# Kernel tuning notes

Hardware: AMD Instinct MI355X
Metric: run time of the kernel (lower is better)

The kernel has to match this reference:

```python
import jax, jax.numpy as jnp
import numpy as np

B, T, D = 4, 4096, 384
H = W = 64
K = 8            # num_clusters
CH = MH = 64     # conv_hidden, mlp_hidden
NL = 4           # num_layers
IN_DIM = D + 2   # use_spatial_pos
RADIUS_FRACTION = 30.0
GRAPH_EPS = 1e-6
SM_LAMBDA = 0.01
FS_LAMBDA = 0.09


def conv2d(x, w, b, groups=1):
    out = jax.lax.conv_general_dilated(x, w, (1, 1), 'SAME',
        dimension_numbers=('NCHW', 'OIHW', 'NCHW'), feature_group_count=groups)
    return out + b[None, :, None, None]


def group_norm(x, g, b, groups, eps=1e-5):
    n, c, h, w = x.shape
    xg = x.reshape(n, groups, c // groups, h, w)
    m = xg.mean(axis=(2, 3, 4), keepdims=True)
    v = xg.var(axis=(2, 3, 4), keepdims=True)
    xn = ((xg - m) * jax.lax.rsqrt(v + eps)).reshape(n, c, h, w)
    return xn * g[None, :, None, None] + b[None, :, None, None]


def layer_norm(x, g, b, eps=1e-5):
    m = x.mean(-1, keepdims=True)
    v = x.var(-1, keepdims=True)
    return (x - m) * jax.lax.rsqrt(v + eps) * g + b


def build_graph():
    # unit-square grid positions; radius graph with self loops; sym normalization
    lin = jnp.linspace(0.0, 1.0, H)
    gy, gx = jnp.meshgrid(lin, lin, indexing='ij')
    pos = jnp.stack([gx.reshape(-1), gy.reshape(-1)], axis=1)  # (T,2)
    r2 = 2.0 / (RADIUS_FRACTION * RADIUS_FRACTION)             # (sqrt(2)/rf)^2
    dx = pos[:, 0][:, None] - pos[:, 0][None, :]
    dy = pos[:, 1][:, None] - pos[:, 1][None, :]
    adj = ((dx * dx + dy * dy) <= r2).astype(jnp.float32)      # includes loop
    deg = adj.sum(1)
    dis = jnp.where(deg > 0, deg ** -0.5, 0.0)
    a_tilde = dis[:, None] * adj * dis[None, :]                # D^-1/2 A D^-1/2
    return pos, a_tilde


def setup_inputs():
    key = jax.random.key(0)
    ks = jax.random.split(key, 16)
    rn = lambda i, s, sc=0.05: jax.random.normal(ks[i], s, dtype=jnp.float32) * sc
    z = lambda s: jnp.zeros(s, jnp.float32)
    o = lambda s: jnp.ones(s, jnp.float32)
    return {
        'token_features': jax.random.normal(ks[0], (B, T, D), dtype=jnp.float32),
        'gcn_w0': rn(1, (IN_DIM, CH)), 'gcn_b0': z((CH,)),
        'gcn_w': rn(2, (NL - 1, CH, CH)), 'gcn_b': z((NL - 1, CH)),
        'ln_g': o((NL, CH)), 'ln_b': z((NL, CH)),
        'res_w': rn(3, (IN_DIM, CH)), 'res_b': z((CH,)),
        'res_ln_g': o((CH,)), 'res_ln_b': z((CH,)),
        'mlp_w1': rn(4, (CH, MH)), 'mlp_b1': z((MH,)),
        'mlp_ln_g': o((MH,)), 'mlp_ln_b': z((MH,)),
        'mlp_w2': rn(5, (MH, K)), 'mlp_b2': z((K,)),
        'sm_w1': rn(6, (K, 1, 3, 3)), 'sm_b1': z((K,)),
        'sm_gn1_g': o((K,)), 'sm_gn1_b': z((K,)),
        'sm_w2': rn(7, (K, 1, 3, 3)), 'sm_b2': z((K,)),
        'sm_gn2_g': o((K,)), 'sm_gn2_b': z((K,)),
        'ec_w1': rn(8, (32, D, 3, 3), 0.02), 'ec_b1': z((32,)),
        'ec_gn_g': o((32,)), 'ec_gn_b': z((32,)),
        'ec_w2': rn(9, (1, 32, 1, 1)), 'ec_b2': z((1,)),
        'k': 8,
    }


def reference(token_features, gcn_w0, gcn_b0, gcn_w, gcn_b, ln_g, ln_b,
              res_w, res_b, res_ln_g, res_ln_b, mlp_w1, mlp_b1, mlp_ln_g,
              mlp_ln_b, mlp_w2, mlp_b2, sm_w1, sm_b1, sm_gn1_g, sm_gn1_b,
              sm_w2, sm_b2, sm_gn2_g, sm_gn2_b, ec_w1, ec_b1, ec_gn_g,
              ec_gn_b, ec_w2, ec_b2, k):
    pos, A = build_graph()

    # ---- feature smoothness loss (edge-aware) ----
    fs = token_features.reshape(B, H, W, D).transpose(0, 3, 1, 2)  # (B,D,H,W)
    e = jax.nn.relu(group_norm(conv2d(fs, ec_w1, ec_b1), ec_gn_g, ec_gn_b, 8))
    ew = jax.nn.sigmoid(conv2d(e, ec_w2, ec_b2))                   # (B,1,H,W)
    gy = fs[:, :, 1:, :] - fs[:, :, :-1, :]
    gx = fs[:, :, :, 1:] - fs[:, :, :, :-1]
    loss_y = (gy * gy * ew[:, :, 1:, :]).mean() / D
    loss_x = (gx * gx * ew[:, :, :, 1:]).mean() / D
    feat_sm = (loss_y + loss_x) / 2

    # ---- GNN pool (batched; adjacency shared across batch) ----
    x = jnp.concatenate(
        [token_features, jnp.broadcast_to(pos[None], (B, T, 2))], axis=-1)
    Ws = [gcn_w0] + [gcn_w[i] for i in range(NL - 1)]
    bs = [gcn_b0] + [gcn_b[i] for i in range(NL - 1)]
    for i in range(NL):
        x_prev = x
        h = jnp.einsum('ts,bsc->btc', A, x @ Ws[i]) + bs[i]  # GCNConv
        h = jax.nn.elu(layer_norm(h, ln_g[i], ln_b[i]))
        if i == 0:
            x_prev = layer_norm(x_prev @ res_w + res_b, res_ln_g, res_ln_b)
        x = h + x_prev
    h1 = jax.nn.elu(layer_norm(x @ mlp_w1 + mlp_b1, mlp_ln_g, mlp_ln_b))
    S = jax.nn.softmax(h1 @ mlp_w2 + mlp_b2, axis=-1)        # (B,T,K)

    # ---- spatial smoothness loss (depthwise convs) ----
    S_sp = S.transpose(0, 2, 1).reshape(B, K, H, W)
    t = jax.nn.relu(group_norm(conv2d(S_sp, sm_w1, sm_b1, groups=K),
                               sm_gn1_g, sm_gn1_b, K))
    S_sm = group_norm(conv2d(t, sm_w2, sm_b2, groups=K), sm_gn2_g, sm_gn2_b, K)
    sm_loss = ((S_sm - S_sp) ** 2).mean(axis=(1, 2, 3))      # (B,)

    # ---- normalized-cut + orthogonality losses ----
    AS = jnp.einsum('ts,bsk->btk', A, S)
    num = jnp.einsum('btk,btk->b', S, AS)
    degA = A.sum(1)
    den = jnp.einsum('btk,t,btk->b', S, degA, S) + GRAPH_EPS
    loss_c = -num / den
    SS = jnp.einsum('btk,btl->bkl', S, S)
    ssn = jnp.sqrt((SS * SS).sum(axis=(1, 2)))
    eyeK = jnp.eye(K, dtype=jnp.float32)
    target = eyeK / (jnp.sqrt(jnp.float32(K)) + GRAPH_EPS)
    diff = SS / (ssn[:, None, None] + GRAPH_EPS) - target[None]
    loss_o = jnp.sqrt((diff * diff).sum(axis=(1, 2)))

    loss = (loss_c + loss_o + SM_LAMBDA * sm_loss).mean() + FS_LAMBDA * feat_sm
    return S, loss
```

## Files before the change

kernel.cpp:

```cpp
#include <hip/hip_runtime.h>
#include <hip/hip_bf16.h>


#define B_ 4
#define T_ 4096
#define D_ 384

typedef __attribute__((ext_vector_type(8))) short short8b;
typedef __attribute__((ext_vector_type(4))) float f32x4;

__device__ __forceinline__ float wred(float v) {
#pragma unroll
  for (int off = 32; off > 0; off >>= 1) v += __shfl_xor(v, off);
  return v;
}

__device__ __forceinline__ void wred2(float& a, float& b) {
#pragma unroll
  for (int off = 32; off > 0; off >>= 1) {
    a += __shfl_xor(a, off);
    b += __shfl_xor(b, off);
  }
}

__device__ __forceinline__ short bf16rne(float f) {
  unsigned u = __float_as_uint(f);
  unsigned r = (u + 0x7FFFu + ((u >> 16) & 1u)) >> 16;
  return (short)r;
}

__device__ __forceinline__ float uval(int i) {
  int c = (i < 2 ? i : 2) + ((63 - i) < 2 ? (63 - i) : 2) + 1;
  return rsqrtf((float)c);
}

__device__ __forceinline__ short8b cvt8(const float* src) {
  float4 f0 = *(const float4*)src;
  float4 f1 = *(const float4*)(src + 4);
  short8b v;
  v[0] = bf16rne(f0.x); v[1] = bf16rne(f0.y);
  v[2] = bf16rne(f0.z); v[3] = bf16rne(f0.w);
  v[4] = bf16rne(f1.x); v[5] = bf16rne(f1.y);
  v[6] = bf16rne(f1.z); v[7] = bf16rne(f1.w);
  return v;
}

struct PGcn {
  const float *feat, *ecw1, *w0, *resw, *resb, *resg, *reslb;
  const float *gw, *gb0, *gb, *lng, *lnb;
  const float *w1, *b1, *mlng, *mlnb, *w2, *b2;
  short *wq, *wb;
  float *accg, *xwA, *xwB, *xbuf, *resbuf, *S, *Sp;
};

struct PLoss {
  const float *S, *Sp;
  const float *smw1, *smb1, *smg1, *smbb1, *smw2, *smb2, *smg2, *smbb2;
  const float *feat;
  const short *wq;
  const float *ecb1;
  float *eraw, *accg;
  const float *gng, *gnb, *ecw2, *ecb2;
  float *ew, *outp;
};


__device__ __forceinline__ void prep_stage(int blk, int tid,
    const float* ecw1, const float* w0, const float* resw,
    short* wq, short* wb, float* accg) {
  if (blk == 0) {
    accg[tid] = 0.f;
    accg[tid + 256] = 0.f;
  }
  if (blk < 432) {
    int idx = blk * 256 + tid;
    int q = idx % 9;
    int rest = idx / 9;
    int d = rest % 384;
    int o = rest / 384;
    wq[((size_t)(q * 32 + o)) * 384 + d] = bf16rne(ecw1[idx]);
  } else {
    int u = (blk - 432) * 256 + tid;
    int l = u & 63, f = (u >> 6) & 7, s = u >> 9;
    int c = f * 16 + (l & 15);
    int k0 = s * 32 + ((l >> 4) << 3);
    const float* src = (c < 64) ? (w0 + c) : (resw + (c - 64));
    short8b v;
#pragma unroll
    for (int j = 0; j < 8; ++j) v[j] = bf16rne(src[(size_t)(k0 + j) * 64]);
    *(short8b*)(wb + (size_t)u * 8) = v;
  }
}

__device__ __forceinline__ void gemm0_stage(char* smem, int blk, int tid,
    const float* feat, const short* wb, const float* w0, const float* resw,
    const float* resb, const float* resg, const float* reslb,
    float* xw, float* res) {
  short8b* Ab8 = (short8b*)smem;
  short8b* Bb8 = (short8b*)(smem + 24576);
  int row0 = blk * 32;
#pragma unroll
  for (int it = 0; it < 6; ++it) {
    int u = it * 256 + tid;
    int l = u & 63, s = (u >> 6) % 12, set = u / 768;
    int row = row0 + set * 16 + (l & 15);
    int k = s * 32 + ((l >> 4) << 3);
    Ab8[(set * 12 + s) * 64 + l] = cvt8(feat + (size_t)row * 384 + k);
  }
  int wid = tid >> 6, lane = tid & 63;
  int rowset = wid & 1, colhalf = wid >> 1;
  const short8b* wb8 = (const short8b*)wb;
  f32x4 acc[4];
#pragma unroll
  for (int f = 0; f < 4; ++f) acc[f] = (f32x4){0.f, 0.f, 0.f, 0.f};
  for (int c = 0; c < 3; ++c) {
    __syncthreads();
#pragma unroll
    for (int it = 0; it < 8; ++it) {
      int u = it * 256 + tid;
      Bb8[u] = wb8[c * 2048 + u];
    }
    __syncthreads();
#pragma unroll
    for (int s = 0; s < 4; ++s) {
      short8b av = Ab8[(rowset * 12 + c * 4 + s) * 64 + lane];
#pragma unroll
      for (int f = 0; f < 4; ++f) {
        short8b bv = Bb8[(s * 8 + colhalf * 4 + f) * 64 + lane];
        acc[f] = __builtin_amdgcn_mfma_f32_16x16x32_bf16(av, bv, acc[f], 0, 0, 0);
      }
    }
  }
  int g = lane >> 4, ln = lane & 15;
  if (colhalf == 0) {
    float pw1[4], pw2[4];
#pragma unroll
    for (int f = 0; f < 4; ++f) {
      int c = f * 16 + ln;
      pw1[f] = w0[384 * 64 + c];
      pw2[f] = w0[385 * 64 + c];
    }
#pragma unroll
    for (int r = 0; r < 4; ++r) {
      int grow = row0 + rowset * 16 + g * 4 + r;
      int t = grow & (T_ - 1);
      float px = (float)(t & 63) * (1.f / 63.f);
      float py = (float)(t >> 6) * (1.f / 63.f);
#pragma unroll
      for (int f = 0; f < 4; ++f)
        xw[(size_t)grow * 64 + f * 16 + ln] = acc[f][r] + px * pw1[f] + py * pw2[f];
    }
  } else {
    float rw1[4], rw2[4], rb[4], rgam[4], rbet[4];
#pragma unroll
    for (int f = 0; f < 4; ++f) {
      int c = f * 16 + ln;
      rw1[f] = resw[384 * 64 + c];
      rw2[f] = resw[385 * 64 + c];
      rb[f] = resb[c]; rgam[f] = resg[c]; rbet[f] = reslb[c];
    }
#pragma unroll
    for (int r = 0; r < 4; ++r) {
      int grow = row0 + rowset * 16 + g * 4 + r;
      int t = grow & (T_ - 1);
      float px = (float)(t & 63) * (1.f / 63.f);
      float py = (float)(t >> 6) * (1.f / 63.f);
      float rv[4];
      float s1 = 0.f, s2 = 0.f;
#pragma unroll
      for (int f = 0; f < 4; ++f) {
        float v = acc[f][r] + px * rw1[f] + py * rw2[f] + rb[f];
        rv[f] = v;
        s1 += v;
        s2 = fmaf(v, v, s2);
      }
#pragma unroll
      for (int off = 1; off < 16; off <<= 1) {
        s1 += __shfl_xor(s1, off);
        s2 += __shfl_xor(s2, off);
      }
      float mean = s1 * (1.f / 64.f);
      float var = s2 * (1.f / 64.f) - mean * mean;
      float inv = rsqrtf(var + 1e-5f);
#pragma unroll
      for (int f = 0; f < 4; ++f)
        res[(size_t)grow * 64 + f * 16 + ln] =
            (rv[f] - mean) * inv * rgam[f] + rbet[f];
    }
  }
}

__device__ __forceinline__ void layer_stage(char* smem, int blk, int tid,
    const float* xw_in, const float* W, const float* bias, const float* lng,
    const float* lnb, const float* resid, float* xout, float* xw_out) {
  float* sx = (float*)smem;
  float* sW = (float*)(smem + 4096);
  int t0 = blk * 16;
  int b = t0 >> 12, i = (t0 >> 6) & 63;
  const float4* w4 = (const float4*)W;
  float4* sW4 = (float4*)sW;
#pragma unroll
  for (int l = 0; l < 4; ++l) sW4[tid + l * 256] = w4[tid + l * 256];
  int c = tid & 63, jg = tid >> 6;
  int jb = (t0 & 63) + jg * 4;
  float ui = uval(i);
  float acc[4];
#pragma unroll
  for (int m = 0; m < 4; ++m) acc[m] = 0.f;
  float uw[8];
#pragma unroll
  for (int d = 0; d < 8; ++d) {
    int jj = jb - 2 + d;
    uw[d] = (jj >= 0 && jj < 64) ? uval(jj) : 0.f;
  }
#pragma unroll
  for (int di = -2; di <= 2; ++di) {
    int ii = i + di;
    if (ii < 0 || ii > 63) continue;
    float wi = uval(ii);
    const float* src = xw_in + ((size_t)((b << 12) + (ii << 6))) * 64 + c;
    float v[8];
#pragma unroll
    for (int d = 0; d < 8; ++d) {
      int jj = jb - 2 + d;
      v[d] = (jj >= 0 && jj < 64) ? src[jj * 64] : 0.f;
    }
#pragma unroll
    for (int m = 0; m < 4; ++m) {
      float t = v[m] * uw[m] + v[m + 1] * uw[m + 1] + v[m + 2] * uw[m + 2] +
                v[m + 3] * uw[m + 3] + v[m + 4] * uw[m + 4];
      acc[m] = fmaf(wi, t, acc[m]);
    }
  }
  float bc = bias[c], gam = lng[c], bet = lnb[c];
#pragma unroll
  for (int m = 0; m < 4; ++m) {
    int lrow = jg * 4 + m;
    float h = ui * uval(jb + m) * acc[m] + bc;
    float s1 = h, s2 = h * h;
    wred2(s1, s2);
    float mean = s1 * (1.f / 64.f);
    float var = s2 * (1.f / 64.f) - mean * mean;
    float n = (h - mean) * rsqrtf(var + 1e-5f) * gam + bet;
    float e = n > 0.f ? n : (expf(n) - 1.f);
    float xv = e + resid[(size_t)(t0 + lrow) * 64 + c];
    xout[(size_t)(t0 + lrow) * 64 + c] = xv;
    sx[lrow * 64 + c] = xv;
  }
  __syncthreads();
  float a[4];
#pragma unroll
  for (int m = 0; m < 4; ++m) a[m] = 0.f;
#pragma unroll
  for (int kq = 0; kq < 16; ++kq) {
    float4 fv[4];
#pragma unroll
    for (int m = 0; m < 4; ++m)
      fv[m] = *(const float4*)&sx[(jg * 4 + m) * 64 + kq * 4];
#pragma unroll
    for (int dk = 0; dk < 4; ++dk) {
      float wv = sW[(kq * 4 + dk) * 64 + c];
#pragma unroll
      for (int m = 0; m < 4; ++m)
        a[m] = fmaf(((const float*)&fv[m])[dk], wv, a[m]);
    }
  }
#pragma unroll
  for (int m = 0; m < 4; ++m)
    xw_out[(size_t)(t0 + jg * 4 + m) * 64 + c] = a[m];
}

__device__ __forceinline__ void st4mlp_stage(char* smem, int blk, int tid,
    const float* xw_in, const float* bias, const float* lng, const float* lnb,
    const float* resid, const float* w1, const float* b1, const float* mlng,
    const float* mlnb, const float* w2, const float* b2, float* S, float* Sp) {
  float* sx = (float*)smem;
  float* sW = (float*)(smem + 8192);
  float* sh = (float*)(smem + 24576);
  int t0 = blk * 32;
  int b = t0 >> 12, i = (t0 >> 6) & 63;
  const float4* w4 = (const float4*)w1;
  float4* sW4 = (float4*)sW;
#pragma unroll
  for (int l = 0; l < 4; ++l) sW4[tid + l * 256] = w4[tid + l * 256];
  int c = tid & 63, jg = tid >> 6;
  int jb = (t0 & 63) + jg * 8;
  float ui = uval(i);
  float acc[8];
#pragma unroll
  for (int m = 0; m < 8; ++m) acc[m] = 0.f;
  float uw[12];
#pragma unroll
  for (int d = 0; d < 12; ++d) {
    int jj = jb - 2 + d;
    uw[d] = (jj >= 0 && jj < 64) ? uval(jj) : 0.f;
  }
#pragma unroll
  for (int di = -2; di <= 2; ++di) {
    int ii = i + di;
    if (ii < 0 || ii > 63) continue;
    float wi = uval(ii);
    const float* src = xw_in + ((size_t)((b << 12) + (ii << 6))) * 64 + c;
    float v[12];
#pragma unroll
    for (int d = 0; d < 12; ++d) {
      int jj = jb - 2 + d;
      v[d] = (jj >= 0 && jj < 64) ? src[jj * 64] : 0.f;
    }
#pragma unroll
    for (int m = 0; m < 8; ++m) {
      float t = v[m] * uw[m] + v[m + 1] * uw[m + 1] + v[m + 2] * uw[m + 2] +
                v[m + 3] * uw[m + 3] + v[m + 4] * uw[m + 4];
      acc[m] = fmaf(wi, t, acc[m]);
    }
  }
  float bc = bias[c], gam = lng[c], bet = lnb[c];
#pragma unroll
  for (int m = 0; m < 8; ++m) {
    int lrow = jg * 8 + m;
    float h = ui * uval(jb + m) * acc[m] + bc;
    float s1 = h, s2 = h * h;
    wred2(s1, s2);
    float mean = s1 * (1.f / 64.f);
    float var = s2 * (1.f / 64.f) - mean * mean;
    float n = (h - mean) * rsqrtf(var + 1e-5f) * gam + bet;
    float e = n > 0.f ? n : (expf(n) - 1.f);
    sx[lrow * 64 + c] = e + resid[(size_t)(t0 + lrow) * 64 + c];
  }
  __syncthreads();
  float a[8];
#pragma unroll
  for (int m = 0; m < 8; ++m) a[m] = 0.f;
#pragma unroll
  for (int kq = 0; kq < 16; ++kq) {
    float4 fv[8];
#pragma unroll
    for (int m = 0; m < 8; ++m)
      fv[m] = *(const float4*)&sx[(jg * 8 + m) * 64 + kq * 4];
#pragma unroll
    for (int dk = 0; dk < 4; ++dk) {
      float wv = sW[(kq * 4 + dk) * 64 + c];
#pragma unroll
      for (int m = 0; m < 8; ++m)
        a[m] = fmaf(((const float*)&fv[m])[dk], wv, a[m]);
    }
  }
  float mb = b1[c], mgam = mlng[c], mbet = mlnb[c];
#pragma unroll
  for (int m = 0; m < 8; ++m) {
    float h = a[m] + mb;
    float s1 = h, s2 = h * h;
    wred2(s1, s2);
    float mean = s1 * (1.f / 64.f);
    float var = s2 * (1.f / 64.f) - mean * mean;
    float n = (h - mean) * rsqrtf(var + 1e-5f) * mgam + mbet;
    sh[(jg * 8 + m) * 64 + c] = n > 0.f ? n : (expf(n) - 1.f);
  }
  __syncthreads();
  int k = tid & 7, j = tid >> 3;
  float lg = b2[k];
#pragma unroll 8
  for (int u = 0; u < 64; ++u) {
    int cc = (u + j * 8) & 63;
    lg = fmaf(sh[j * 64 + cc], w2[cc * 8 + k], lg);
  }
  float mx = lg;
  mx = fmaxf(mx, __shfl_xor(mx, 1));
  mx = fmaxf(mx, __shfl_xor(mx, 2));
  mx = fmaxf(mx, __shfl_xor(mx, 4));
  float ex = expf(lg - mx);
  float sum = ex;
  sum += __shfl_xor(sum, 1);
  sum += __shfl_xor(sum, 2);
  sum += __shfl_xor(sum, 4);
  float val = ex / sum;
  int grow = t0 + j;
  int t = grow & (T_ - 1);
  S[(size_t)grow * 8 + k] = val;
  Sp[((size_t)((b << 3) + k) << 12) + t] = val;
}

__device__ __forceinline__ void cut_stage(char* smem, int blk, int tid,
    const float* S, float* accg) {
  {
    int k = tid & 7;
    int tl = tid >> 3;
    int gid = blk * 32 + tl;
    int b = gid >> 12, t = gid & (T_ - 1);
    int i = t >> 6, j = t & 63;
    float ui = uval(i), uj = uval(j);
    float as = 0.f, sui = 0.f, suj = 0.f;
#pragma unroll
    for (int di = -2; di <= 2; ++di) {
      int ii = i + di;
      if (ii < 0 || ii > 63) continue;
      float wi = uval(ii);
      sui += wi;
#pragma unroll
      for (int dj = -2; dj <= 2; ++dj) {
        int jj = j + dj;
        if (jj < 0 || jj > 63) continue;
        as = fmaf(wi * uval(jj),
                  S[((size_t)((b << 12) + (ii << 6) + jj)) * 8 + k], as);
      }
    }
#pragma unroll
    for (int dj = -2; dj <= 2; ++dj) {
      int jj = j + dj;
      if (jj >= 0 && jj <= 63) suj += uval(jj);
    }
    as *= ui * uj;
    float sv = S[(size_t)gid * 8 + k];
    float degA = ui * uj * sui * suj;
    float numv = sv * as, denv = sv * sv * degA;
    wred2(numv, denv);
    float* lds = (float*)smem;
    int wid = tid >> 6, lane = tid & 63;
    if (lane == 0) { lds[wid * 2] = numv; lds[wid * 2 + 1] = denv; }
    __syncthreads();
    if (tid == 0) {
      int slot = b * 4 + (blk & 3);
      atomicAdd(&accg[slot], lds[0] + lds[2] + lds[4] + lds[6]);
      atomicAdd(&accg[16 + slot], lds[1] + lds[3] + lds[5] + lds[7]);
    }
  }
  if (blk < 32) {
    __syncthreads();
    int b = blk >> 3, chunk = blk & 7;
    int wid = tid >> 6, lane = tid & 63;
    int kk = lane >> 3, ll = lane & 7;
    int t0 = chunk * 512 + wid * 128;
    float a = 0.f;
    const float* Sb = S + ((size_t)b << 12) * 8;
    for (int it = 0; it < 128; ++it) {
      const float* sr = Sb + (size_t)(t0 + it) * 8;
      a = fmaf(sr[kk], sr[ll], a);
    }
    float* lds2 = (float*)smem;
    lds2[tid] = a;
    __syncthreads();
    if (tid < 64) {
      float s = lds2[tid] + lds2[tid + 64] + lds2[tid + 128] + lds2[tid + 192];
      atomicAdd(&accg[128 + b * 64 + tid], s);
    }
  }
}

__device__ __forceinline__ void sm_stage(char* smem, int bk, int tid,
    const float* Sp, const float* w1, const float* b1, const float* g1,
    const float* bb1, const float* w2, const float* b2, const float* g2,
    const float* bb2, float* accg) {
  float* p0 = (float*)smem;
  float* p1 = p0 + 4096;
  float* red = p1 + 4096;
  int b = bk >> 3, k = bk & 7;
  const float4* src = (const float4*)(Sp + (size_t)bk * 4096);
  float4* d0 = (float4*)p0;
  for (int i2 = tid; i2 < 1024; i2 += 256) d0[i2] = src[i2];
  float W1[9], W2[9];
#pragma unroll
  for (int q = 0; q < 9; ++q) { W1[q] = w1[k * 9 + q]; W2[q] = w2[k * 9 + q]; }
  __syncthreads();
  int wid = tid >> 6, lane = tid & 63;
  float y[16];
  float s1 = 0.f, s2 = 0.f;
#pragma unroll
  for (int v = 0; v < 16; ++v) {
    int p = v * 256 + tid;
    int i2 = p >> 6, j2 = p & 63;
    float a = b1[k];
#pragma unroll
    for (int dy = 0; dy < 3; ++dy) {
      int ii = i2 + dy - 1;
      if (ii < 0 || ii > 63) continue;
#pragma unroll
      for (int dx = 0; dx < 3; ++dx) {
        int jj = j2 + dx - 1;
        if (jj < 0 || jj > 63) continue;
        a = fmaf(W1[dy * 3 + dx], p0[(ii << 6) + jj], a);
      }
    }
    y[v] = a;
    s1 += a;
    s2 = fmaf(a, a, s2);
  }
  wred2(s1, s2);
  if (lane == 0) { red[wid * 2] = s1; red[wid * 2 + 1] = s2; }
  __syncthreads();
  float mean = (red[0] + red[2] + red[4] + red[6]) * (1.f / 4096.f);
  float var = (red[1] + red[3] + red[5] + red[7]) * (1.f / 4096.f) - mean * mean;
  float inv = rsqrtf(var + 1e-5f) * g1[k];
  float sh = bb1[k];
  __syncthreads();
#pragma unroll
  for (int v = 0; v < 16; ++v) {
    int p = v * 256 + tid;
    p1[p] = fmaxf((y[v] - mean) * inv + sh, 0.f);
  }
  __syncthreads();
  s1 = 0.f; s2 = 0.f;
#pragma unroll
  for (int v = 0; v < 16; ++v) {
    int p = v * 256 + tid;
    int i2 = p >> 6, j2 = p & 63;
    float a = b2[k];
#pragma unroll
    for (int dy = 0; dy < 3; ++dy) {
      int ii = i2 + dy - 1;
      if (ii < 0 || ii > 63) continue;
#pragma unroll
      for (int dx = 0; dx < 3; ++dx) {
        int jj = j2 + dx - 1;
        if (jj < 0 || jj > 63) continue;
        a = fmaf(W2[dy * 3 + dx], p1[(ii << 6) + jj], a);
      }
    }
    y[v] = a;
    s1 += a;
    s2 = fmaf(a, a, s2);
  }
  wred2(s1, s2);
  if (lane == 0) { red[wid * 2] = s1; red[wid * 2 + 1] = s2; }
  __syncthreads();
  float mean2 = (red[0] + red[2] + red[4] + red[6]) * (1.f / 4096.f);
  float var2 = (red[1] + red[3] + red[5] + red[7]) * (1.f / 4096.f) - mean2 * mean2;
  float inv2 = rsqrtf(var2 + 1e-5f) * g2[k];
  float sh2 = bb2[k];
  float sd = 0.f;
#pragma unroll
  for (int v = 0; v < 16; ++v) {
    int p = v * 256 + tid;
    float sm = (y[v] - mean2) * inv2 + sh2;
    float dd = sm - p0[p];
    sd = fmaf(dd, dd, sd);
  }
  sd = wred(sd);
  __syncthreads();
  if (lane == 0) red[wid] = sd;
  __syncthreads();
  if (tid == 0)
    atomicAdd(&accg[384 + b * 2 + (bk & 1)],
              (red[0] + red[1] + red[2] + red[3]) * (1.f / 32768.f));
}

__device__ __forceinline__ void ecconv_stage(char* smem, int blk2, int tid,
    const float* feat, const short* wq, const float* ecb1, float* eraw,
    float* accg) {
  short* Abuf = (short*)smem;
  short* Wbuf = Abuf + 6432;
  float* sW1 = (float*)(Wbuf + 9216);
  float* sW2 = sW1 + 128;
  int b = blk2 >> 6, i = blk2 & 63;
  int wid = tid >> 6, lane = tid & 63;
  int m = lane & 15, kg = lane >> 4;
  if (tid < 36) {
    int zkg = tid & 3, sl = (tid >> 2) % 3, r = tid / 12;
    int slot = sl == 0 ? 0 : (sl == 1 ? 65 : 66);
    *(short8b*)&Abuf[(r * 67 + slot) * 32 + zkg * 8] = (short8b)0;
  }
  f32x4 acc0 = {0.f, 0.f, 0.f, 0.f};
  f32x4 acc1 = {0.f, 0.f, 0.f, 0.f};
  int abase = (wid * 16 + m) * 32 + kg * 8;
  int bbase = m * 32 + kg * 8;
  for (int c = 0; c < 12; ++c) {
    __syncthreads();
#pragma unroll
    for (int s = 0; s < 3; ++s) {
      int cid = tid + (s << 8);
      int akg = cid & 3, px = (cid >> 2) & 63, r = cid >> 8;
      int ii = i + r - 1;
      short8b v = (short8b)0;
      if (ii >= 0 && ii < 64)
        v = cvt8(feat + ((size_t)((b << 12) + (ii << 6) + px)) * D_ + c * 32 +
                 akg * 8);
      *(short8b*)&Abuf[(r * 67 + px + 1) * 32 + akg * 8] = v;
    }
    for (int l = tid; l < 1152; l += 256) {
      int wkg = l & 3, oo = (l >> 2) & 31, q = l >> 7;
      short8b wv =
          *(const short8b*)(wq + ((size_t)(q * 32 + oo)) * D_ + c * 32 + wkg * 8);
      *(short8b*)&Wbuf[(q * 32 + oo) * 32 + wkg * 8] = wv;
    }
    __syncthreads();
#pragma unroll
    for (int q = 0; q < 9; ++q) {
      short8b av = *(const short8b*)&Abuf[abase + ((q / 3) * 67 + (q % 3)) * 32];
      short8b bv0 = *(const short8b*)&Wbuf[bbase + q * 1024];
      short8b bv1 = *(const short8b*)&Wbuf[bbase + q * 1024 + 512];
      acc0 = __builtin_amdgcn_mfma_f32_16x16x32_bf16(av, bv0, acc0, 0, 0, 0);
      acc1 = __builtin_amdgcn_mfma_f32_16x16x32_bf16(av, bv1, acc1, 0, 0, 0);
    }
  }
  int o0 = m, o1 = 16 + m;
  float bs0 = ecb1[o0], bs1 = ecb1[o1];
  float s1a = 0.f, s2a = 0.f, s1b = 0.f, s2b = 0.f;
  int jbase = wid * 16 + kg * 4;
#pragma unroll
  for (int rg = 0; rg < 4; ++rg) {
    float v0 = acc0[rg] + bs0;
    float v1 = acc1[rg] + bs1;
    int j = jbase + rg;
    size_t px = ((size_t)((b << 12) + (i << 6) + j)) * 32;
    eraw[px + o0] = v0;
    eraw[px + o1] = v1;
    s1a += v0; s2a = fmaf(v0, v0, s2a);
    s1b += v1; s2b = fmaf(v1, v1, s2b);
  }
  s1a += __shfl_xor(s1a, 16); s1a += __shfl_xor(s1a, 32);
  s2a += __shfl_xor(s2a, 16); s2a += __shfl_xor(s2a, 32);
  s1b += __shfl_xor(s1b, 16); s1b += __shfl_xor(s1b, 32);
  s2b += __shfl_xor(s2b, 16); s2b += __shfl_xor(s2b, 32);
  if (lane < 16) {
    sW1[wid * 32 + lane] = s1a; sW2[wid * 32 + lane] = s2a;
    sW1[wid * 32 + lane + 16] = s1b; sW2[wid * 32 + lane + 16] = s2b;
  }
  __syncthreads();
  if (tid < 32) {
    float t1 = sW1[tid] + sW1[32 + tid] + sW1[64 + tid] + sW1[96 + tid];
    float t2 = sW2[tid] + sW2[32 + tid] + sW2[64 + tid] + sW2[96 + tid];
    t1 += __shfl_xor(t1, 1); t1 += __shfl_xor(t1, 2);
    t2 += __shfl_xor(t2, 1); t2 += __shfl_xor(t2, 2);
    if ((tid & 3) == 0) {
      atomicAdd(&accg[64 + b * 16 + (tid >> 2) * 2], t1);
      atomicAdd(&accg[64 + b * 16 + (tid >> 2) * 2 + 1], t2);
    }
  }
}

__device__ __forceinline__ void ecfinal_stage(char* smem, int blk, int tid,
    const float* eraw, const float* accg, const float* gng, const float* gnb,
    const float* w2, const float* b2, float* ew) {
  float* st = (float*)smem;
  int idx = blk * 256 + tid;
  int b = idx >> 12;
  if (tid < 16) st[tid] = accg[64 + b * 16 + tid];
  __syncthreads();
  float a = b2[0];
  const float4* er = (const float4*)(eraw + (size_t)idx * 32);
#pragma unroll
  for (int oq = 0; oq < 8; ++oq) {
    float mean = st[oq * 2] * (1.f / 16384.f);
    float var = st[oq * 2 + 1] * (1.f / 16384.f) - mean * mean;
    float inv = rsqrtf(var + 1e-5f);
    float4 e = er[oq];
    int o = oq * 4;
    float v0 = (e.x - mean) * inv * gng[o + 0] + gnb[o + 0];
    float v1 = (e.y - mean) * inv * gng[o + 1] + gnb[o + 1];
    float v2 = (e.z - mean) * inv * gng[o + 2] + gnb[o + 2];
    float v3 = (e.w - mean) * inv * gng[o + 3] + gnb[o + 3];
    a = fmaf(fmaxf(v0, 0.f), w2[o + 0], a);
    a = fmaf(fmaxf(v1, 0.f), w2[o + 1], a);
    a = fmaf(fmaxf(v2, 0.f), w2[o + 2], a);
    a = fmaf(fmaxf(v3, 0.f), w2[o + 3], a);
  }
  ew[idx] = 1.f / (1.f + expf(-a));
}

__device__ __forceinline__ void fsloss_stage(char* smem, int blk, int tid,
    const float* feat, const float* ew, float* accg) {
  float sy = 0.f, sx = 0.f;
  const int N = B_ * T_ * 96;
  for (int idx = blk * 256 + tid; idx < N; idx += 512 * 256) {
    int d4 = idx % 96;
    int rt = idx / 96;
    int t = rt & (T_ - 1);
    int i = t >> 6, j = t & 63;
    const float4* fp = (const float4*)(feat + (size_t)rt * D_) + d4;
    float4 f0 = *fp;
    if (i < 63) {
      float4 f1 = fp[64 * 96];
      float w = ew[rt + 64];
      float a = f1.x - f0.x, bq = f1.y - f0.y, cz = f1.z - f0.z, d = f1.w - f0.w;
      sy += w * (a * a + bq * bq + cz * cz + d * d);
    }
    if (j < 63) {
      float4 f1 = fp[96];
      float w = ew[rt + 1];
      float a = f1.x - f0.x, bq = f1.y - f0.y, cz = f1.z - f0.z, d = f1.w - f0.w;
      sx += w * (a * a + bq * bq + cz * cz + d * d);
    }
  }
  wred2(sy, sx);
  float* lds = (float*)smem;
  int wid = tid >> 6, lane = tid & 63;
  if (lane == 0) { lds[wid * 2] = sy; lds[wid * 2 + 1] = sx; }
  __syncthreads();
  if (tid == 0) {
    int slot = 32 + (blk & 15) * 2;
    atomicAdd(&accg[slot], lds[0] + lds[2] + lds[4] + lds[6]);
    atomicAdd(&accg[slot + 1], lds[1] + lds[3] + lds[5] + lds[7]);
  }
}

__device__ __forceinline__ void final_stage(const float* accg, float* out) {
  float total = 0.f;
  for (int b = 0; b < 4; ++b) {
    const float* SSb = accg + 128 + b * 64;
    float ssq = 0.f;
    for (int v = 0; v < 64; ++v) ssq += SSb[v] * SSb[v];
    float ssn = sqrtf(ssq);
    float tgt = 1.f / (sqrtf(8.f) + 1e-6f);
    float inv = 1.f / (ssn + 1e-6f);
    float lo = 0.f;
    for (int kk = 0; kk < 8; ++kk)
      for (int ll = 0; ll < 8; ++ll) {
        float dd = SSb[kk * 8 + ll] * inv - (kk == ll ? tgt : 0.f);
        lo += dd * dd;
      }
    lo = sqrtf(lo);
    float num = accg[b * 4] + accg[b * 4 + 1] + accg[b * 4 + 2] + accg[b * 4 + 3];
    float den = accg[16 + b * 4] + accg[16 + b * 4 + 1] + accg[16 + b * 4 + 2] +
                accg[16 + b * 4 + 3];
    float lc = -num / (den + 1e-6f);
    float smv = accg[384 + b * 2] + accg[385 + b * 2];
    total += lc + lo + 0.01f * smv;
  }
  total *= 0.25f;
  float fsy = 0.f, fsx = 0.f;
  for (int s = 0; s < 16; ++s) { fsy += accg[32 + s * 2]; fsx += accg[33 + s * 2]; }
  const float cnt = 4.f * 384.f * 63.f * 64.f;
  float ly = fsy / cnt * (1.f / 384.f);
  float lx = fsx / cnt * (1.f / 384.f);
  out[131072] = total + 0.09f * 0.5f * (ly + lx);
}


__global__ __launch_bounds__(256) void k_prep(PGcn p) {
  prep_stage(blockIdx.x, threadIdx.x, p.ecw1, p.w0, p.resw, p.wq, p.wb, p.accg);
}

__global__ __launch_bounds__(256) void k_mix1(PGcn g, PLoss l) {
  __shared__ __align__(16) char smem[57344];
  if (blockIdx.x < 256)
    ecconv_stage(smem, blockIdx.x, threadIdx.x, l.feat, l.wq, l.ecb1, l.eraw,
                 l.accg);
  else
    gemm0_stage(smem, blockIdx.x - 256, threadIdx.x, g.feat, g.wb, g.w0, g.resw,
                g.resb, g.resg, g.reslb, g.xwA, g.resbuf);
}

__global__ __launch_bounds__(256) void k_mix2(PGcn g, PLoss l) {
  __shared__ __align__(16) char smem[20480];
  if (blockIdx.x < 64)
    ecfinal_stage(smem, blockIdx.x, threadIdx.x, l.eraw, l.accg, l.gng, l.gnb,
                  l.ecw2, l.ecb2, l.ew);
  else
    layer_stage(smem, blockIdx.x - 64, threadIdx.x, g.xwA, g.gw, g.gb0, g.lng,
                g.lnb, g.resbuf, g.xbuf, g.xwB);
}

__global__ __launch_bounds__(256) void k_mix3(PGcn g, PLoss l) {
  __shared__ __align__(16) char smem[20480];
  if (blockIdx.x < 512)
    fsloss_stage(smem, blockIdx.x, threadIdx.x, l.feat, l.ew, l.accg);
  else
    layer_stage(smem, blockIdx.x - 512, threadIdx.x, g.xwB, g.gw + 4096, g.gb,
                g.lng + 64, g.lnb + 64, g.xbuf, g.xbuf, g.xwA);
}

__global__ __launch_bounds__(256) void k_layer2(PGcn p) {
  __shared__ __align__(16) char smem[20480];
  layer_stage(smem, blockIdx.x, threadIdx.x, p.xwA, p.gw + 8192, p.gb + 64,
              p.lng + 128, p.lnb + 128, p.xbuf, p.xbuf, p.xwB);
}

__global__ __launch_bounds__(256) void k_st4mlp(PGcn p) {
  __shared__ __align__(16) char smem[32768];
  st4mlp_stage(smem, blockIdx.x, threadIdx.x, p.xwB, p.gb + 128, p.lng + 192,
               p.lnb + 192, p.xbuf, p.w1, p.b1, p.mlng, p.mlnb, p.w2, p.b2,
               p.S, p.Sp);
}

__global__ __launch_bounds__(256) void k_cutsm(PLoss p) {
  __shared__ __align__(16) char smem[32832];
  if (blockIdx.x < 512)
    cut_stage(smem, blockIdx.x, threadIdx.x, p.S, p.accg);
  else
    sm_stage(smem, blockIdx.x - 512, threadIdx.x, p.Sp, p.smw1, p.smb1, p.smg1,
             p.smbb1, p.smw2, p.smb2, p.smg2, p.smbb2, p.accg);
}

__global__ void k_final(PLoss p) {
  if (threadIdx.x == 0 && blockIdx.x == 0) final_stage(p.accg, p.outp);
}


extern "C" void kernel_launch(void* const* d_in, const int* in_sizes, int n_in,
                              void* d_out, int out_size, void* d_ws, size_t ws_size,
                              hipStream_t stream) {
  const float* feat = (const float*)d_in[0];
  const float* gcn_w0 = (const float*)d_in[1];
  const float* gcn_b0 = (const float*)d_in[2];
  const float* gcn_w = (const float*)d_in[3];
  const float* gcn_b = (const float*)d_in[4];
  const float* ln_g = (const float*)d_in[5];
  const float* ln_b = (const float*)d_in[6];
  const float* res_w = (const float*)d_in[7];
  const float* res_b = (const float*)d_in[8];
  const float* res_ln_g = (const float*)d_in[9];
  const float* res_ln_b = (const float*)d_in[10];
  const float* mlp_w1 = (const float*)d_in[11];
  const float* mlp_b1 = (const float*)d_in[12];
  const float* mlp_ln_g = (const float*)d_in[13];
  const float* mlp_ln_b = (const float*)d_in[14];
  const float* mlp_w2 = (const float*)d_in[15];
  const float* mlp_b2 = (const float*)d_in[16];
  const float* sm_w1 = (const float*)d_in[17];
  const float* sm_b1 = (const float*)d_in[18];
  const float* sm_g1 = (const float*)d_in[19];
  const float* sm_bb1 = (const float*)d_in[20];
  const float* sm_w2 = (const float*)d_in[21];
  const float* sm_b2 = (const float*)d_in[22];
  const float* sm_g2 = (const float*)d_in[23];
  const float* sm_bb2 = (const float*)d_in[24];
  const float* ec_w1 = (const float*)d_in[25];
  const float* ec_b1 = (const float*)d_in[26];
  const float* ec_gn_g = (const float*)d_in[27];
  const float* ec_gn_b = (const float*)d_in[28];
  const float* ec_w2 = (const float*)d_in[29];
  const float* ec_b2 = (const float*)d_in[30];

  float* out = (float*)d_out;
  float* ws = (float*)d_ws;
  float* acc = ws;
  float* xwA = ws + 512;
  float* xwB = xwA + 1048576;
  float* xbuf = xwB + 1048576;
  float* resbuf = xbuf + 1048576;
  float* Sp = resbuf + 1048576;
  float* eraw = Sp + 131072;
  float* ew = eraw + 524288;
  short* wqb = (short*)(ew + 16384);
  short* wb = wqb + 110592;
  float* S = out;

  PGcn pg = {feat, ec_w1, gcn_w0, res_w, res_b, res_ln_g, res_ln_b,
             gcn_w, gcn_b0, gcn_b, ln_g, ln_b,
             mlp_w1, mlp_b1, mlp_ln_g, mlp_ln_b, mlp_w2, mlp_b2,
             wqb, wb, acc, xwA, xwB, xbuf, resbuf, S, Sp};
  PLoss pl = {S, Sp, sm_w1, sm_b1, sm_g1, sm_bb1, sm_w2, sm_b2, sm_g2, sm_bb2,
              feat, wqb, ec_b1, eraw, acc, ec_gn_g, ec_gn_b, ec_w2, ec_b2, ew,
              out};

  k_prep<<<456, 256, 0, stream>>>(pg);
  k_mix1<<<768, 256, 0, stream>>>(pg, pl);
  k_mix2<<<1088, 256, 0, stream>>>(pg, pl);
  k_mix3<<<1536, 256, 0, stream>>>(pg, pl);
  k_layer2<<<1024, 256, 0, stream>>>(pg);
  k_st4mlp<<<512, 256, 0, stream>>>(pg);
  k_cutsm<<<544, 256, 0, stream>>>(pl);
  k_final<<<1, 64, 0, stream>>>(pl);
}
```

Measured before the change: 129.0 us.

## Read MFMA weights from global directly, cache bf16 features, remap conv blocks

Both the ecconv and gemm0 stages stop staging weight tiles in LDS and load the MFMA B operands straight from global memory (L2-resident). This cuts shared memory use and removes a sync per chunk. The ecconv A buffer gets a padded row stride of 40 to avoid bank conflicts, and conv block indices are remapped to interleave batches. gemm0 also writes a bf16 copy of the features, which the feature-smoothness loss then reads at half the bytes. The trade-off is lower precision in that loss and more scattered global loads for the weights.

```diff
diff --git a/kernel.cpp b/kernel.cpp
--- a/kernel.cpp
+++ b/kernel.cpp
@@ -27,6 +27,10 @@
   unsigned u = __float_as_uint(f);
   unsigned r = (u + 0x7FFFu + ((u >> 16) & 1u)) >> 16;
   return (short)r;
+}
+
+__device__ __forceinline__ float bf2f(short s) {
+  return __uint_as_float(((unsigned)(unsigned short)s) << 16);
 }
 
 __device__ __forceinline__ float uval(int i) {
@@ -49,7 +53,7 @@
   const float *feat, *ecw1, *w0, *resw, *resb, *resg, *reslb;
   const float *gw, *gb0, *gb, *lng, *lnb;
   const float *w1, *b1, *mlng, *mlnb, *w2, *b2;
-  short *wq, *wb;
+  short *wq, *wb, *fb;
   float *accg, *xwA, *xwB, *xbuf, *resbuf, *S, *Sp;
 };
 
@@ -57,7 +61,7 @@
   const float *S, *Sp;
   const float *smw1, *smb1, *smg1, *smbb1, *smw2, *smb2, *smg2, *smbb2;
   const float *feat;
-  const short *wq;
+  const short *wq, *fb;
   const float *ecb1;
   float *eraw, *accg;
   const float *gng, *gnb, *ecw2, *ecb2;
@@ -93,11 +97,10 @@
 }
 
 __device__ __forceinline__ void gemm0_stage(char* smem, int blk, int tid,
-    const float* feat, const short* wb, const float* w0, const float* resw,
-    const float* resb, const float* resg, const float* reslb,
-    float* xw, float* res) {
+    const float* feat, const short* wb, short* fbout, const float* w0,
+    const float* resw, const float* resb, const float* resg,
+    const float* reslb, float* xw, float* res) {
   short8b* Ab8 = (short8b*)smem;
-  short8b* Bb8 = (short8b*)(smem + 24576);
   int row0 = blk * 32;
 #pragma unroll
   for (int it = 0; it < 6; ++it) {
@@ -105,30 +108,24 @@
     int l = u & 63, s = (u >> 6) % 12, set = u / 768;
     int row = row0 + set * 16 + (l & 15);
     int k = s * 32 + ((l >> 4) << 3);
-    Ab8[(set * 12 + s) * 64 + l] = cvt8(feat + (size_t)row * 384 + k);
-  }
+    short8b v = cvt8(feat + (size_t)row * 384 + k);
+    Ab8[(set * 12 + s) * 64 + l] = v;
+    *(short8b*)(fbout + (size_t)row * 384 + k) = v;
+  }
+  __syncthreads();
   int wid = tid >> 6, lane = tid & 63;
   int rowset = wid & 1, colhalf = wid >> 1;
   const short8b* wb8 = (const short8b*)wb;
   f32x4 acc[4];
 #pragma unroll
   for (int f = 0; f < 4; ++f) acc[f] = (f32x4){0.f, 0.f, 0.f, 0.f};
-  for (int c = 0; c < 3; ++c) {
-    __syncthreads();
-#pragma unroll
-    for (int it = 0; it < 8; ++it) {
-      int u = it * 256 + tid;
-      Bb8[u] = wb8[c * 2048 + u];
-    }
-    __syncthreads();
-#pragma unroll
-    for (int s = 0; s < 4; ++s) {
-      short8b av = Ab8[(rowset * 12 + c * 4 + s) * 64 + lane];
-#pragma unroll
-      for (int f = 0; f < 4; ++f) {
-        short8b bv = Bb8[(s * 8 + colhalf * 4 + f) * 64 + lane];
-        acc[f] = __builtin_amdgcn_mfma_f32_16x16x32_bf16(av, bv, acc[f], 0, 0, 0);
-      }
+#pragma unroll
+  for (int s = 0; s < 12; ++s) {
+    short8b av = Ab8[(rowset * 12 + s) * 64 + lane];
+#pragma unroll
+    for (int f = 0; f < 4; ++f) {
+      short8b bv = wb8[((size_t)(s * 8 + colhalf * 4 + f)) * 64 + lane];
+      acc[f] = __builtin_amdgcn_mfma_f32_16x16x32_bf16(av, bv, acc[f], 0, 0, 0);
     }
   }
   int g = lane >> 4, ln = lane & 15;
@@ -547,8 +544,7 @@
     const float* feat, const short* wq, const float* ecb1, float* eraw,
     float* accg) {
   short* Abuf = (short*)smem;
-  short* Wbuf = Abuf + 6432;
-  float* sW1 = (float*)(Wbuf + 9216);
+  float* sW1 = (float*)(smem + 16128);
   float* sW2 = sW1 + 128;
   int b = blk2 >> 6, i = blk2 & 63;
   int wid = tid >> 6, lane = tid & 63;
@@ -556,12 +552,11 @@
   if (tid < 36) {
     int zkg = tid & 3, sl = (tid >> 2) % 3, r = tid / 12;
     int slot = sl == 0 ? 0 : (sl == 1 ? 65 : 66);
-    *(short8b*)&Abuf[(r * 67 + slot) * 32 + zkg * 8] = (short8b)0;
+    *(short8b*)&Abuf[(r * 67 + slot) * 40 + zkg * 8] = (short8b)0;
   }
   f32x4 acc0 = {0.f, 0.f, 0.f, 0.f};
   f32x4 acc1 = {0.f, 0.f, 0.f, 0.f};
-  int abase = (wid * 16 + m) * 32 + kg * 8;
-  int bbase = m * 32 + kg * 8;
+  int abase = (wid * 16 + m) * 40 + kg * 8;
   for (int c = 0; c < 12; ++c) {
     __syncthreads();
 #pragma unroll
@@ -573,20 +568,15 @@
       if (ii >= 0 && ii < 64)
         v = cvt8(feat + ((size_t)((b << 12) + (ii << 6) + px)) * D_ + c * 32 +
                  akg * 8);
-      *(short8b*)&Abuf[(r * 67 + px + 1) * 32 + akg * 8] = v;
-    }
-    for (int l = tid; l < 1152; l += 256) {
-      int wkg = l & 3, oo = (l >> 2) & 31, q = l >> 7;
-      short8b wv =
-          *(const short8b*)(wq + ((size_t)(q * 32 + oo)) * D_ + c * 32 + wkg * 8);
-      *(short8b*)&Wbuf[(q * 32 + oo) * 32 + wkg * 8] = wv;
+      *(short8b*)&Abuf[(r * 67 + px + 1) * 40 + akg * 8] = v;
     }
     __syncthreads();
 #pragma unroll
     for (int q = 0; q < 9; ++q) {
-      short8b av = *(const short8b*)&Abuf[abase + ((q / 3) * 67 + (q % 3)) * 32];
-      short8b bv0 = *(const short8b*)&Wbuf[bbase + q * 1024];
-      short8b bv1 = *(const short8b*)&Wbuf[bbase + q * 1024 + 512];
+      short8b av = *(const short8b*)&Abuf[abase + ((q / 3) * 67 + (q % 3)) * 40];
+      const short* wqb = wq + ((size_t)(q * 32 + m)) * 384 + c * 32 + kg * 8;
+      short8b bv0 = *(const short8b*)wqb;
+      short8b bv1 = *(const short8b*)(wqb + 16 * 384);
       acc0 = __builtin_amdgcn_mfma_f32_16x16x32_bf16(av, bv0, acc0, 0, 0, 0);
       acc1 = __builtin_amdgcn_mfma_f32_16x16x32_bf16(av, bv1, acc1, 0, 0, 0);
     }
@@ -657,27 +647,37 @@
 }
 
 __device__ __forceinline__ void fsloss_stage(char* smem, int blk, int tid,
-    const float* feat, const float* ew, float* accg) {
+    const short* fb, const float* ew, float* accg) {
   float sy = 0.f, sx = 0.f;
-  const int N = B_ * T_ * 96;
+  const int N = B_ * T_ * 48;
   for (int idx = blk * 256 + tid; idx < N; idx += 512 * 256) {
-    int d4 = idx % 96;
-    int rt = idx / 96;
+    int d8 = idx % 48;
+    int rt = idx / 48;
     int t = rt & (T_ - 1);
     int i = t >> 6, j = t & 63;
-    const float4* fp = (const float4*)(feat + (size_t)rt * D_) + d4;
-    float4 f0 = *fp;
+    const short8b* fp = (const short8b*)(fb + (size_t)rt * D_) + d8;
+    short8b f0 = *fp;
     if (i < 63) {
-      float4 f1 = fp[64 * 96];
+      short8b f1 = fp[64 * 48];
       float w = ew[rt + 64];
-      float a = f1.x - f0.x, bq = f1.y - f0.y, cz = f1.z - f0.z, d = f1.w - f0.w;
-      sy += w * (a * a + bq * bq + cz * cz + d * d);
+      float a = 0.f;
+#pragma unroll
+      for (int u = 0; u < 8; ++u) {
+        float d = bf2f(f1[u]) - bf2f(f0[u]);
+        a = fmaf(d, d, a);
+      }
+      sy += w * a;
     }
     if (j < 63) {
-      float4 f1 = fp[96];
+      short8b f1 = fp[48];
       float w = ew[rt + 1];
-      float a = f1.x - f0.x, bq = f1.y - f0.y, cz = f1.z - f0.z, d = f1.w - f0.w;
-      sx += w * (a * a + bq * bq + cz * cz + d * d);
+      float a = 0.f;
+#pragma unroll
+      for (int u = 0; u < 8; ++u) {
+        float d = bf2f(f1[u]) - bf2f(f0[u]);
+        a = fmaf(d, d, a);
+      }
+      sx += w * a;
     }
   }
   wred2(sy, sx);
@@ -730,13 +730,14 @@
 }
 
 __global__ __launch_bounds__(256) void k_mix1(PGcn g, PLoss l) {
-  __shared__ __align__(16) char smem[57344];
-  if (blockIdx.x < 256)
-    ecconv_stage(smem, blockIdx.x, threadIdx.x, l.feat, l.wq, l.ecb1, l.eraw,
-                 l.accg);
-  else
-    gemm0_stage(smem, blockIdx.x - 256, threadIdx.x, g.feat, g.wb, g.w0, g.resw,
-                g.resb, g.resg, g.reslb, g.xwA, g.resbuf);
+  __shared__ __align__(16) char smem[24576];
+  if (blockIdx.x < 256) {
+    int lb = (blockIdx.x & 7) * 32 + (blockIdx.x >> 3);
+    ecconv_stage(smem, lb, threadIdx.x, l.feat, l.wq, l.ecb1, l.eraw, l.accg);
+  } else {
+    gemm0_stage(smem, blockIdx.x - 256, threadIdx.x, g.feat, g.wb, g.fb, g.w0,
+                g.resw, g.resb, g.resg, g.reslb, g.xwA, g.resbuf);
+  }
 }
 
 __global__ __launch_bounds__(256) void k_mix2(PGcn g, PLoss l) {
@@ -752,7 +753,7 @@
 __global__ __launch_bounds__(256) void k_mix3(PGcn g, PLoss l) {
   __shared__ __align__(16) char smem[20480];
   if (blockIdx.x < 512)
-    fsloss_stage(smem, blockIdx.x, threadIdx.x, l.feat, l.ew, l.accg);
+    fsloss_stage(smem, blockIdx.x, threadIdx.x, l.fb, l.ew, l.accg);
   else
     layer_stage(smem, blockIdx.x - 512, threadIdx.x, g.xwB, g.gw + 4096, g.gb,
                 g.lng + 64, g.lnb + 64, g.xbuf, g.xbuf, g.xwA);
@@ -832,15 +833,16 @@
   float* ew = eraw + 524288;
   short* wqb = (short*)(ew + 16384);
   short* wb = wqb + 110592;
+  short* fb = wb + 49152;
   float* S = out;
 
   PGcn pg = {feat, ec_w1, gcn_w0, res_w, res_b, res_ln_g, res_ln_b,
              gcn_w, gcn_b0, gcn_b, ln_g, ln_b,
              mlp_w1, mlp_b1, mlp_ln_g, mlp_ln_b, mlp_w2, mlp_b2,
-             wqb, wb, acc, xwA, xwB, xbuf, resbuf, S, Sp};
+             wqb, wb, fb, acc, xwA, xwB, xbuf, resbuf, S, Sp};
   PLoss pl = {S, Sp, sm_w1, sm_b1, sm_g1, sm_bb1, sm_w2, sm_b2, sm_g2, sm_bb2,
-              feat, wqb, ec_b1, eraw, acc, ec_gn_g, ec_gn_b, ec_w2, ec_b2, ew,
-              out};
+              feat, wqb, fb, ec_b1, eraw, acc, ec_gn_g, ec_gn_b, ec_w2, ec_b2,
+              ew, out};
 
   k_prep<<<456, 256, 0, stream>>>(pg);
   k_mix1<<<768, 256, 0, stream>>>(pg, pl);
```

Result: slower. 138.1 us (+7.1%).
